# Kernel tuning notes

Measured on AMD Instinct MI355X. Metric: run time of the kernel, lower is better.

## Reference

```python
import jax, jax.numpy as jnp
import numpy as np

N = 100000      # hits
P = 512         # particle ids (0 = noise, skipped)
D = 8           # condensation-space dim
Q_MIN = 0.01
REPULSION_SCALING = 10.0


def setup_inputs() -> dict:
    key = jax.random.key(0)
    k1, k2, k3, k4, k5 = jax.random.split(key, 5)
    w = jax.random.normal(k1, (N,), dtype=jnp.float32)
    # beta in (0, 0.95) so arctanh stays well-conditioned
    beta = jax.random.uniform(k2, (N,), dtype=jnp.float32) * 0.95
    x = jax.random.normal(k3, (N, D), dtype=jnp.float32)
    y = jax.random.normal(k4, (N,), dtype=jnp.float32)
    particle_id = jax.random.randint(k5, (N,), 0, P)
    return {"w": w, "beta": beta, "x": x, "y": y, "particle_id": particle_id}


def _safe_sqrt(s):
    # sqrt with zero (sub)gradient at 0, matching torch.norm's behavior at 0
    pos = s > 0
    return jnp.where(pos, jnp.sqrt(jnp.where(pos, s, 1.0)), 0.0)


def _condensation_loss(beta, x, particle_id):
    n = beta.shape[0]
    q = jnp.arctanh(beta) ** 2 + Q_MIN                     # [N]
    # per-particle condensation point: hit with max q (torch.argmax -> first)
    q_max = jax.ops.segment_max(q, particle_id, num_segments=P)          # [P]
    counts = jax.ops.segment_sum(jnp.ones_like(q), particle_id, num_segments=P)
    is_max = q == q_max[particle_id]
    cand = jnp.where(is_max, jnp.arange(n), n)
    alpha_idx = jnp.clip(jax.ops.segment_min(cand, particle_id, num_segments=P), 0, n - 1)
    valid = (counts > 0) & (jnp.arange(P) != 0)            # skip noise pid 0 and absent pids
    q_alpha = jnp.where(valid, q_max, 0.0)                 # [P], sanitized (-inf for empty segs)
    x_alpha = x[alpha_idx]                                  # [P, D]
    # squared distances [N, P] via GEMM (avoids [N, P, D] intermediate)
    sq = (jnp.sum(x * x, axis=1, keepdims=True)
          - 2.0 * (x @ x_alpha.T)
          + jnp.sum(x_alpha * x_alpha, axis=1)[None, :])
    sq = jnp.maximum(sq, 0.0)
    dist = _safe_sqrt(sq)
    va = sq * q_alpha[None, :]                              # attractive potential
    vr = jnp.maximum(1.0 - dist, 0.0) * q_alpha[None, :]    # repulsive hinge
    M = (particle_id[:, None] == jnp.arange(P)[None, :]).astype(x.dtype)  # [N, P]
    per_p = jnp.mean(q[:, None] * (M * va + REPULSION_SCALING * (1.0 - M) * vr), axis=0)  # [P]
    return jnp.sum(jnp.where(valid, per_p, 0.0))


def reference(w, beta, x, y, particle_id):
    return _condensation_loss(beta, x, particle_id)
```

## Files before the change

kernel.cpp:

```cpp
#include <hip/hip_runtime.h>

#define P_IDS 512
#define DIM 8
#define QMIN 0.01f
#define REP 10.0f
#define A_BLOCKS 128
#define CHUNK 128

typedef unsigned long long ull;

__launch_bounds__(256)
__global__ void stageA_kernel(const float* __restrict__ beta,
                              const int* __restrict__ pid,
                              float* __restrict__ q_out,
                              ull* __restrict__ tables,
                              int n) {
    __shared__ ull s_keys[P_IDS];
    for (int t = threadIdx.x; t < P_IDS; t += 256) s_keys[t] = 0ULL;
    __syncthreads();
    for (int i = blockIdx.x * 256 + threadIdx.x; i < n; i += gridDim.x * 256) {
        float b = beta[i];
        float at = 0.5f * logf((1.0f + b) / (1.0f - b));
        float q = fmaf(at, at, QMIN);
        q_out[i] = q;
        ull key = ((ull)__float_as_uint(q) << 32) |
                  (ull)(unsigned int)(~(unsigned int)i);
        atomicMax(&s_keys[pid[i]], key);
    }
    __syncthreads();
    for (int t = threadIdx.x; t < P_IDS; t += 256)
        tables[blockIdx.x * P_IDS + t] = s_keys[t];
}

__launch_bounds__(64)
__global__ void stageB_kernel(const ull* __restrict__ tables,
                              const float* __restrict__ x,
                              float2* __restrict__ meta,
                              float* __restrict__ x_alpha,
                              float* __restrict__ out) {
    int p = blockIdx.x * 64 + threadIdx.x;
    ull k = 0ULL;
    for (int t = 0; t < A_BLOCKS; ++t) {
        ull v = tables[t * P_IDS + p];
        k = (v > k) ? v : k;
    }
    bool valid = (k != 0ULL) && (p != 0);
    float qa = valid ? __uint_as_float((unsigned int)(k >> 32)) : 0.0f;
    int idx = valid ? (int)(~(unsigned int)(k & 0xFFFFFFFFull)) : 0;
    float xa2 = 0.0f;
#pragma unroll
    for (int d = 0; d < DIM; ++d) {
        float v = x[idx * DIM + d];
        x_alpha[p * DIM + d] = v;
        xa2 = fmaf(v, v, xa2);
    }
    meta[p] = make_float2(qa, xa2);
    if (p == 0) out[0] = 0.0f;
}

__launch_bounds__(256)
__global__ void loss_kernel(const float* __restrict__ x,
                            const float* __restrict__ q,
                            const int* __restrict__ pid,
                            const float2* __restrict__ meta,
                            const float* __restrict__ x_alpha,
                            float* __restrict__ out,
                            int n) {
    __shared__ float  s_xa[CHUNK * DIM];
    __shared__ float2 s_meta[CHUNK];
    int chunk = blockIdx.x & 3;
    int hb    = blockIdx.x >> 2;
    int p0    = chunk * CHUNK;

    if (threadIdx.x < CHUNK * DIM / 4)
        ((float4*)s_xa)[threadIdx.x] =
            ((const float4*)(x_alpha + p0 * DIM))[threadIdx.x];
    if (threadIdx.x < CHUNK) s_meta[threadIdx.x] = meta[p0 + threadIdx.x];
    __syncthreads();

    int i = hb * 256 + threadIdx.x;
    float partial = 0.0f;
    if (i < n) {
        const float4* x4 = (const float4*)x;
        float4 a = x4[i * 2];
        float4 c = x4[i * 2 + 1];
        float xi[DIM] = {a.x, a.y, a.z, a.w, c.x, c.y, c.z, c.w};
        float xi2 = 0.0f;
#pragma unroll
        for (int d = 0; d < DIM; ++d) xi2 = fmaf(xi[d], xi[d], xi2);
        float qi = q[i];
        int myj = pid[i] - p0;
        float acc = 0.0f;
#pragma unroll 4
        for (int j = 0; j < CHUNK; ++j) {
            float2 m = s_meta[j];
            const float* xa = &s_xa[j * DIM];
            float dot = 0.0f;
#pragma unroll
            for (int d = 0; d < DIM; ++d) dot = fmaf(xi[d], xa[d], dot);
            float sq = fmaxf(fmaf(-2.0f, dot, xi2 + m.y), 0.0f);
            float dist = __builtin_amdgcn_sqrtf(sq);
            float vr = fmaxf(1.0f - dist, 0.0f);
            float t = (j == myj) ? sq : REP * vr;
            acc = fmaf(t, m.x, acc);
        }
        partial = qi * acc;
    }

#pragma unroll
    for (int off = 32; off > 0; off >>= 1)
        partial += __shfl_down(partial, off, 64);
    __shared__ float s_red[4];
    if ((threadIdx.x & 63) == 0) s_red[threadIdx.x >> 6] = partial;
    __syncthreads();
    if (threadIdx.x == 0) {
        float s = (s_red[0] + s_red[1] + s_red[2] + s_red[3]) / (float)n;
        atomicAdd(out, s);
    }
}

extern "C" void kernel_launch(void* const* d_in, const int* in_sizes, int n_in,
                              void* d_out, int out_size, void* d_ws, size_t ws_size,
                              hipStream_t stream) {
    int n = in_sizes[0];
    const float* beta = (const float*)d_in[1];
    const float* x    = (const float*)d_in[2];
    const int*   pid  = (const int*)d_in[4];
    float* out = (float*)d_out;

    char* ws = (char*)d_ws;
    size_t tab_bytes = (size_t)A_BLOCKS * P_IDS * sizeof(ull);
    size_t q_bytes   = (((size_t)n * 4) + 255) & ~(size_t)255;
    ull*    tables  = (ull*)ws;
    float*  q       = (float*)(ws + tab_bytes);
    float2* meta    = (float2*)(ws + tab_bytes + q_bytes);
    float*  x_alpha = (float*)(ws + tab_bytes + q_bytes + P_IDS * sizeof(float2));

    stageA_kernel<<<A_BLOCKS, 256, 0, stream>>>(beta, pid, q, tables, n);
    stageB_kernel<<<P_IDS / 64, 64, 0, stream>>>(tables, x, meta, x_alpha, out);
    int hit_blocks = (n + 255) / 256;
    loss_kernel<<<hit_blocks * 4, 256, 0, stream>>>(x, q, pid, meta, x_alpha, out, n);
}
```

Baseline: 101.8 us.

## Register-block hits per thread, skip hinge when far, restructure stage A/B reductions

The loss kernel now keeps four hits per thread in registers and reuses each shared-memory condensation point across them. It uses smaller particle chunks. When no hit in the wavefront lies within unit distance, the sqrt and hinge work is skipped. The same-particle attractive term moves out of the inner loop into a single correction per hit. Stage A now uses one block per 256 hits, which produces about 391 partial tables (~1.6 MB of workspace). Stage B now does one block per particle and reduces those tables with a wavefront shuffle. The larger table raises memory traffic in stages A and B.

```diff
diff --git a/kernel.cpp b/kernel.cpp
--- a/kernel.cpp
+++ b/kernel.cpp
@@ -4,8 +4,10 @@
 #define DIM 8
 #define QMIN 0.01f
 #define REP 10.0f
-#define A_BLOCKS 128
-#define CHUNK 128
+#define CHUNK 64
+#define NCHUNK (P_IDS / CHUNK)
+#define HPT 4
+#define HB (256 * HPT)
 
 typedef unsigned long long ull;
 
@@ -16,46 +18,57 @@
                               ull* __restrict__ tables,
                               int n) {
     __shared__ ull s_keys[P_IDS];
-    for (int t = threadIdx.x; t < P_IDS; t += 256) s_keys[t] = 0ULL;
+    s_keys[threadIdx.x] = 0ULL;
+    s_keys[threadIdx.x + 256] = 0ULL;
     __syncthreads();
-    for (int i = blockIdx.x * 256 + threadIdx.x; i < n; i += gridDim.x * 256) {
+    int i = blockIdx.x * 256 + threadIdx.x;
+    if (i < n) {
         float b = beta[i];
         float at = 0.5f * logf((1.0f + b) / (1.0f - b));
-        float q = fmaf(at, at, QMIN);
-        q_out[i] = q;
-        ull key = ((ull)__float_as_uint(q) << 32) |
+        float qv = fmaf(at, at, QMIN);
+        q_out[i] = qv;
+        ull key = ((ull)__float_as_uint(qv) << 32) |
                   (ull)(unsigned int)(~(unsigned int)i);
         atomicMax(&s_keys[pid[i]], key);
     }
     __syncthreads();
-    for (int t = threadIdx.x; t < P_IDS; t += 256)
-        tables[blockIdx.x * P_IDS + t] = s_keys[t];
+    ull* dst = tables + (size_t)blockIdx.x * P_IDS;
+    dst[threadIdx.x] = s_keys[threadIdx.x];
+    dst[threadIdx.x + 256] = s_keys[threadIdx.x + 256];
 }
 
 __launch_bounds__(64)
-__global__ void stageB_kernel(const ull* __restrict__ tables,
+__global__ void stageB_kernel(const ull* __restrict__ tables, int ntab,
                               const float* __restrict__ x,
                               float2* __restrict__ meta,
                               float* __restrict__ x_alpha,
                               float* __restrict__ out) {
-    int p = blockIdx.x * 64 + threadIdx.x;
+    int p = blockIdx.x;
     ull k = 0ULL;
-    for (int t = 0; t < A_BLOCKS; ++t) {
-        ull v = tables[t * P_IDS + p];
+    for (int t = threadIdx.x; t < ntab; t += 64) {
+        ull v = tables[(size_t)t * P_IDS + p];
         k = (v > k) ? v : k;
     }
-    bool valid = (k != 0ULL) && (p != 0);
-    float qa = valid ? __uint_as_float((unsigned int)(k >> 32)) : 0.0f;
-    int idx = valid ? (int)(~(unsigned int)(k & 0xFFFFFFFFull)) : 0;
-    float xa2 = 0.0f;
 #pragma unroll
-    for (int d = 0; d < DIM; ++d) {
-        float v = x[idx * DIM + d];
-        x_alpha[p * DIM + d] = v;
-        xa2 = fmaf(v, v, xa2);
+    for (int off = 32; off > 0; off >>= 1) {
+        ull o = __shfl_down(k, off, 64);
+        k = (o > k) ? o : k;
     }
-    meta[p] = make_float2(qa, xa2);
-    if (p == 0) out[0] = 0.0f;
+    if (threadIdx.x == 0) {
+        bool valid = (k != 0ULL) && (p != 0);
+        float qa = valid ? __uint_as_float((unsigned int)(k >> 32)) : 0.0f;
+        int idx = valid ? (int)(~(unsigned int)(k & 0xFFFFFFFFull)) : 0;
+        float4 a = ((const float4*)x)[idx * 2];
+        float4 b = ((const float4*)x)[idx * 2 + 1];
+        float xa2 = a.x * a.x;
+        xa2 = fmaf(a.y, a.y, xa2); xa2 = fmaf(a.z, a.z, xa2); xa2 = fmaf(a.w, a.w, xa2);
+        xa2 = fmaf(b.x, b.x, xa2); xa2 = fmaf(b.y, b.y, xa2); xa2 = fmaf(b.z, b.z, xa2);
+        xa2 = fmaf(b.w, b.w, xa2);
+        ((float4*)x_alpha)[p * 2] = a;
+        ((float4*)x_alpha)[p * 2 + 1] = b;
+        meta[p] = make_float2(qa, xa2);
+        if (p == 0) out[0] = 0.0f;
+    }
 }
 
 __launch_bounds__(256)
@@ -68,43 +81,75 @@
                             int n) {
     __shared__ float  s_xa[CHUNK * DIM];
     __shared__ float2 s_meta[CHUNK];
-    int chunk = blockIdx.x & 3;
-    int hb    = blockIdx.x >> 2;
+    int chunk = blockIdx.x & (NCHUNK - 1);
+    int hb    = blockIdx.x / NCHUNK;
     int p0    = chunk * CHUNK;
-
     if (threadIdx.x < CHUNK * DIM / 4)
         ((float4*)s_xa)[threadIdx.x] =
             ((const float4*)(x_alpha + p0 * DIM))[threadIdx.x];
     if (threadIdx.x < CHUNK) s_meta[threadIdx.x] = meta[p0 + threadIdx.x];
     __syncthreads();
 
-    int i = hb * 256 + threadIdx.x;
+    float xi[HPT][DIM], xi2[HPT], qi[HPT], acc[HPT];
+    int   myj[HPT];
+    int base = hb * HB + threadIdx.x;
+#pragma unroll
+    for (int h = 0; h < HPT; ++h) {
+        int i = base + h * 256;
+        bool act = i < n;
+        int ii = act ? i : 0;
+        float4 v0 = ((const float4*)x)[ii * 2];
+        float4 v1 = ((const float4*)x)[ii * 2 + 1];
+        xi[h][0] = v0.x; xi[h][1] = v0.y; xi[h][2] = v0.z; xi[h][3] = v0.w;
+        xi[h][4] = v1.x; xi[h][5] = v1.y; xi[h][6] = v1.z; xi[h][7] = v1.w;
+        float s = 0.0f;
+#pragma unroll
+        for (int d = 0; d < DIM; ++d) s = fmaf(xi[h][d], xi[h][d], s);
+        xi2[h] = s;
+        qi[h]  = act ? q[ii] : 0.0f;
+        myj[h] = act ? (pid[ii] - p0) : -1;
+        acc[h] = 0.0f;
+    }
+
+    for (int j = 0; j < CHUNK; ++j) {
+        float2 m  = s_meta[j];
+        float4 a0 = ((const float4*)s_xa)[j * 2];
+        float4 a1 = ((const float4*)s_xa)[j * 2 + 1];
+        float sq[HPT];
+#pragma unroll
+        for (int h = 0; h < HPT; ++h) {
+            float dot = xi[h][0] * a0.x;
+            dot = fmaf(xi[h][1], a0.y, dot); dot = fmaf(xi[h][2], a0.z, dot);
+            dot = fmaf(xi[h][3], a0.w, dot); dot = fmaf(xi[h][4], a1.x, dot);
+            dot = fmaf(xi[h][5], a1.y, dot); dot = fmaf(xi[h][6], a1.z, dot);
+            dot = fmaf(xi[h][7], a1.w, dot);
+            sq[h] = fmaxf(fmaf(-2.0f, dot, xi2[h] + m.y), 0.0f);
+        }
+        float mn = fminf(fminf(sq[0], sq[1]), fminf(sq[2], sq[3]));
+        if (__any(mn < 1.0f)) {
+#pragma unroll
+            for (int h = 0; h < HPT; ++h) {
+                float vr = fmaxf(1.0f - __builtin_amdgcn_sqrtf(sq[h]), 0.0f);
+                acc[h] = fmaf(vr, m.x, acc[h]);
+            }
+        }
+    }
+
     float partial = 0.0f;
-    if (i < n) {
-        const float4* x4 = (const float4*)x;
-        float4 a = x4[i * 2];
-        float4 c = x4[i * 2 + 1];
-        float xi[DIM] = {a.x, a.y, a.z, a.w, c.x, c.y, c.z, c.w};
-        float xi2 = 0.0f;
 #pragma unroll
-        for (int d = 0; d < DIM; ++d) xi2 = fmaf(xi[d], xi[d], xi2);
-        float qi = q[i];
-        int myj = pid[i] - p0;
-        float acc = 0.0f;
-#pragma unroll 4
-        for (int j = 0; j < CHUNK; ++j) {
+    for (int h = 0; h < HPT; ++h) {
+        float t = REP * acc[h];
+        int j = myj[h];
+        if (j >= 0 && j < CHUNK) {
             float2 m = s_meta[j];
-            const float* xa = &s_xa[j * DIM];
-            float dot = 0.0f;
+            float dot = xi[h][0] * s_xa[j * DIM + 0];
 #pragma unroll
-            for (int d = 0; d < DIM; ++d) dot = fmaf(xi[d], xa[d], dot);
-            float sq = fmaxf(fmaf(-2.0f, dot, xi2 + m.y), 0.0f);
-            float dist = __builtin_amdgcn_sqrtf(sq);
-            float vr = fmaxf(1.0f - dist, 0.0f);
-            float t = (j == myj) ? sq : REP * vr;
-            acc = fmaf(t, m.x, acc);
+            for (int d = 1; d < DIM; ++d) dot = fmaf(xi[h][d], s_xa[j * DIM + d], dot);
+            float sq = fmaxf(fmaf(-2.0f, dot, xi2[h] + m.y), 0.0f);
+            float vr = fmaxf(1.0f - __builtin_amdgcn_sqrtf(sq), 0.0f);
+            t += m.x * (sq - REP * vr);
         }
-        partial = qi * acc;
+        partial = fmaf(qi[h], t, partial);
     }
 
 #pragma unroll
@@ -113,10 +158,8 @@
     __shared__ float s_red[4];
     if ((threadIdx.x & 63) == 0) s_red[threadIdx.x >> 6] = partial;
     __syncthreads();
-    if (threadIdx.x == 0) {
-        float s = (s_red[0] + s_red[1] + s_red[2] + s_red[3]) / (float)n;
-        atomicAdd(out, s);
-    }
+    if (threadIdx.x == 0)
+        atomicAdd(out, (s_red[0] + s_red[1] + s_red[2] + s_red[3]) / (float)n);
 }
 
 extern "C" void kernel_launch(void* const* d_in, const int* in_sizes, int n_in,
@@ -128,16 +171,18 @@
     const int*   pid  = (const int*)d_in[4];
     float* out = (float*)d_out;
 
+    int a_blocks = (n + 255) / 256;
     char* ws = (char*)d_ws;
-    size_t tab_bytes = (size_t)A_BLOCKS * P_IDS * sizeof(ull);
-    size_t q_bytes   = (((size_t)n * 4) + 255) & ~(size_t)255;
+    size_t tab_bytes = (size_t)a_blocks * P_IDS * sizeof(ull);
+    tab_bytes = (tab_bytes + 255) & ~(size_t)255;
+    size_t q_bytes = (((size_t)n * 4) + 255) & ~(size_t)255;
     ull*    tables  = (ull*)ws;
     float*  q       = (float*)(ws + tab_bytes);
     float2* meta    = (float2*)(ws + tab_bytes + q_bytes);
     float*  x_alpha = (float*)(ws + tab_bytes + q_bytes + P_IDS * sizeof(float2));
 
-    stageA_kernel<<<A_BLOCKS, 256, 0, stream>>>(beta, pid, q, tables, n);
-    stageB_kernel<<<P_IDS / 64, 64, 0, stream>>>(tables, x, meta, x_alpha, out);
-    int hit_blocks = (n + 255) / 256;
-    loss_kernel<<<hit_blocks * 4, 256, 0, stream>>>(x, q, pid, meta, x_alpha, out, n);
+    stageA_kernel<<<a_blocks, 256, 0, stream>>>(beta, pid, q, tables, n);
+    stageB_kernel<<<P_IDS, 64, 0, stream>>>(tables, a_blocks, x, meta, x_alpha, out);
+    int hit_blocks = (n + HB - 1) / HB;
+    loss_kernel<<<hit_blocks * NCHUNK, 256, 0, stream>>>(x, q, pid, meta, x_alpha, out, n);
 }
```

After: 96.58 us. -5.2%, faster.
